# Kernel tuning notes

Measured on AMD Instinct MI355X. Metric: run time of the kernel, lower is better.

The kernel has to match this reference:

```python
import jax, jax.numpy as jnp
import numpy as np

N_NODES = 100000
N_EDGES = 1600000
IN_DIM, HID_DIM, OUT_DIM = 128, 64, 40


def setup_inputs() -> dict:
    key = jax.random.key(0)
    k1, k2, k3, k4, k5, k6 = jax.random.split(key, 6)
    x = jax.random.normal(k1, (N_NODES, IN_DIM), dtype=jnp.float32)
    edge_index = jax.random.randint(k2, (2, N_EDGES), 0, N_NODES, dtype=jnp.int64)
    W1 = jax.random.normal(k3, (IN_DIM, HID_DIM), dtype=jnp.float32) * 0.05
    b1 = jnp.zeros((HID_DIM,), dtype=jnp.float32)
    W2 = jax.random.normal(k4, (HID_DIM, OUT_DIM), dtype=jnp.float32) * 0.05
    b2 = jnp.zeros((OUT_DIM,), dtype=jnp.float32)
    return {"x": x, "edge_index": edge_index, "W1": W1, "b1": b1, "W2": W2, "b2": b2}


def gcn_conv(x, src, dst, W, b, n_nodes):
    """PyG GCNConv: linear -> symmetric-normalized aggregation (with self loops) -> + bias."""
    h = x @ W                                                # [N, C_out]
    # degree of targets, including the implicit self loop (weight 1 each)
    deg = jax.ops.segment_sum(jnp.ones_like(dst, dtype=h.dtype), dst,
                              num_segments=n_nodes) + 1.0    # [N]
    dinv = jax.lax.rsqrt(deg)                                # deg >= 1, always valid
    norm = dinv[src] * dinv[dst]                             # [E] edge norm coefficients
    msg = h[src] * norm[:, None]                             # [E, C_out] gather + scale
    agg = jax.ops.segment_sum(msg, dst, num_segments=n_nodes)
    # self-loop contribution: norm_ii = dinv_i * dinv_i
    agg = agg + h * (dinv * dinv)[:, None]
    return agg + b


def reference(x, edge_index, W1, b1, W2, b2):
    src, dst = edge_index[0], edge_index[1]  # source_to_target flow (PyG default)
    n = x.shape[0]
    h = gcn_conv(x, src, dst, W1, b1, n)
    h = jax.nn.relu(h)
    # dropout is identity in eval mode (training=False)
    out = gcn_conv(h, src, dst, W2, b2, n)
    return out
```

## Files before the change

kernel.cpp:

```cpp
#include <hip/hip_runtime.h>
#include <math.h>

#define N_NODES 100000
#define N_EDGES 1600000
#define IN_DIM 128
#define HID_DIM 64
#define OUT_DIM 40

#define NPAD 102400

#define BUCKET_SHIFT 7
#define BUCKET_NODES 128
#define N_BUCKETS 782
#define CHUNK 2048
#define N_CHUNKS 784

typedef _Float16 f16;
typedef _Float16 f16x2 __attribute__((ext_vector_type(2)));
typedef _Float16 f16x4 __attribute__((ext_vector_type(4)));
typedef _Float16 f16x8 __attribute__((ext_vector_type(8)));
typedef float f32x4 __attribute__((ext_vector_type(4)));


__global__ __launch_bounds__(256) void hist_kernel(const int* __restrict__ dst,
                                                   int* __restrict__ hist,
                                                   const float* __restrict__ W1,
                                                   const float* __restrict__ W2,
                                                   f16* __restrict__ w1f,
                                                   f16* __restrict__ w2f) {
    __shared__ int lh[N_BUCKETS];
    int c = blockIdx.x;
    int t = threadIdx.x;
    if (c < N_CHUNKS) {
        for (int b = t; b < N_BUCKETS; b += 256) lh[b] = 0;
        __syncthreads();
        int e0 = c * CHUNK;
        for (int i = t; i < CHUNK; i += 256) {
            int e = e0 + i;
            if (e < N_EDGES) atomicAdd(&lh[dst[e] >> BUCKET_SHIFT], 1);
        }
        __syncthreads();
        for (int b = t; b < N_BUCKETS; b += 256) hist[b * N_CHUNKS + c] = lh[b];
    } else if (c == N_CHUNKS) {
        for (int g = t; g < 1024; g += 256) {
            int f = g >> 6, L = g & 63;
            int s = f >> 2, cc = f & 3;
            int q = L >> 4, n = L & 15;
            f16x8 v;
#pragma unroll
            for (int j = 0; j < 8; ++j)
                v[j] = (f16)W1[(32 * s + 8 * q + j) * HID_DIM + 16 * cc + n];
            *(f16x8*)&w1f[(size_t)g * 8] = v;
        }
    } else {
        for (int g = t; g < 384; g += 256) {
            int f = g >> 6, L = g & 63;
            int s = f / 3, cc = f % 3;
            int q = L >> 4, n = L & 15;
            int col = 16 * cc + n;
            f16x8 v;
#pragma unroll
            for (int j = 0; j < 8; ++j)
                v[j] = (col < OUT_DIM) ? (f16)W2[(32 * s + 8 * q + j) * OUT_DIM + col] : (f16)0.f;
            *(f16x8*)&w2f[(size_t)g * 8] = v;
        }
    }
}

__global__ __launch_bounds__(256) void scan_chunks_kernel(const int* __restrict__ hist,
                                                          int* __restrict__ base,
                                                          int* __restrict__ bucketTotal) {
    __shared__ int lds[256];
    int b = blockIdx.x;
    int t = threadIdx.x;
    int v[4];
    int s = 0;
    for (int k = 0; k < 4; ++k) {
        int c = 4 * t + k;
        int cv = (c < N_CHUNKS) ? hist[b * N_CHUNKS + c] : 0;
        v[k] = s;
        s += cv;
    }
    lds[t] = s;
    __syncthreads();
    for (int off = 1; off < 256; off <<= 1) {
        int val = (t >= off) ? lds[t - off] : 0;
        __syncthreads();
        lds[t] += val;
        __syncthreads();
    }
    int excl = (t == 0) ? 0 : lds[t - 1];
    for (int k = 0; k < 4; ++k) {
        int c = 4 * t + k;
        if (c < N_CHUNKS) base[b * N_CHUNKS + c] = excl + v[k];
    }
    if (t == 255) bucketTotal[b] = lds[255];
}

__global__ __launch_bounds__(256) void scan_buckets_kernel(const int* __restrict__ bucketTotal,
                                                           int* __restrict__ bucketBase) {
    __shared__ int lds[256];
    int t = threadIdx.x;
    int v[4];
    int s = 0;
    for (int k = 0; k < 4; ++k) {
        int b = 4 * t + k;
        int cv = (b < N_BUCKETS) ? bucketTotal[b] : 0;
        v[k] = s;
        s += cv;
    }
    lds[t] = s;
    __syncthreads();
    for (int off = 1; off < 256; off <<= 1) {
        int val = (t >= off) ? lds[t - off] : 0;
        __syncthreads();
        lds[t] += val;
        __syncthreads();
    }
    int excl = (t == 0) ? 0 : lds[t - 1];
    for (int k = 0; k < 4; ++k) {
        int b = 4 * t + k;
        if (b < N_BUCKETS) bucketBase[b] = excl + v[k];
    }
}

__global__ __launch_bounds__(256) void scatter_kernel(const int* __restrict__ src,
                                                      const int* __restrict__ dst,
                                                      const int* __restrict__ base,
                                                      const int* __restrict__ bucketBase,
                                                      int* __restrict__ stage) {
    __shared__ int lbase[N_BUCKETS];
    __shared__ int lcnt[N_BUCKETS];
    int bid = blockIdx.x;
    int chunk = (bid & 7) * 98 + (bid >> 3);
    int t = threadIdx.x;
    for (int b = t; b < N_BUCKETS; b += 256) {
        lbase[b] = base[b * N_CHUNKS + chunk] + bucketBase[b];
        lcnt[b] = 0;
    }
    __syncthreads();
    int e0 = chunk * CHUNK;
    for (int i = t; i < CHUNK; i += 256) {
        int e = e0 + i;
        if (e < N_EDGES) {
            int d = dst[e];
            int b = d >> BUCKET_SHIFT;
            int pos = lbase[b] + atomicAdd(&lcnt[b], 1);
            stage[pos] = ((d & (BUCKET_NODES - 1)) << 17) | src[e];
        }
    }
}

__global__ __launch_bounds__(256) void place_kernel(const int* __restrict__ stage,
                                                    const int* __restrict__ bucketBase,
                                                    int* __restrict__ csr,
                                                    int* __restrict__ row_start,
                                                    int* __restrict__ cnt,
                                                    float* __restrict__ dinv) {
    __shared__ int lhist[BUCKET_NODES];
    __shared__ int lscan[BUCKET_NODES];
    __shared__ int lstart[BUCKET_NODES];
    __shared__ int lcur[BUCKET_NODES];
    int b = blockIdx.x;
    int t = threadIdx.x;
    int est = bucketBase[b];
    int een = (b == N_BUCKETS - 1) ? N_EDGES : bucketBase[b + 1];
    if (t < BUCKET_NODES) { lhist[t] = 0; lcur[t] = 0; }
    __syncthreads();
    for (int e = est + t; e < een; e += 256) atomicAdd(&lhist[stage[e] >> 17], 1);
    __syncthreads();
    if (t < BUCKET_NODES) lscan[t] = lhist[t];
    __syncthreads();
    for (int off = 1; off < BUCKET_NODES; off <<= 1) {
        int val = (t >= off && t < BUCKET_NODES) ? lscan[t - off] : 0;
        __syncthreads();
        if (t < BUCKET_NODES) lscan[t] += val;
        __syncthreads();
    }
    if (t < BUCKET_NODES) {
        int myexcl = (t == 0) ? 0 : lscan[t - 1];
        lstart[t] = est + myexcl;
        int node = (b << BUCKET_SHIFT) + t;
        if (node < N_NODES) {
            row_start[node] = est + myexcl;
            cnt[node] = lhist[t];
            dinv[node] = rsqrtf((float)lhist[t] + 1.0f);
        }
    }
    __syncthreads();
    for (int e = est + t; e < een; e += 256) {
        int rec = stage[e];
        int dl = rec >> 17;
        int pos = lstart[dl] + atomicAdd(&lcur[dl], 1);
        csr[pos] = rec & 0x1FFFF;
    }
}

__global__ __launch_bounds__(256) void gemm1_kernel(const float* __restrict__ x,
                                                    const f16* __restrict__ w1f,
                                                    const float* __restrict__ dinv,
                                                    f16* __restrict__ h1p) {
    __shared__ f16 aT[1088 * 8];
    int t = threadIdx.x;
    int nodeBase = blockIdx.x * 64;
    int L = t & 63;

    const f16x8* w1f8 = (const f16x8*)w1f;
    f16x8 bfrag[16];
#pragma unroll
    for (int f = 0; f < 16; ++f) bfrag[f] = w1f8[f * 64 + L];

#pragma unroll
    for (int i = 0; i < 8; ++i) {
        int idx = i * 256 + t;
        int node = idx >> 5;
        int col4 = idx & 31;
        int gnode = nodeBase + node;
        if (gnode >= N_NODES) gnode = N_NODES - 1;
        float4 v = *(const float4*)&x[(size_t)gnode * IN_DIM + col4 * 4];
        int w = node >> 4, m = node & 15;
        int s = col4 >> 3, q = (col4 >> 1) & 3, j0 = (col4 & 1) * 4;
        f16x4 h;
        h.x = (f16)v.x; h.y = (f16)v.y; h.z = (f16)v.z; h.w = (f16)v.w;
        int idx16 = (w * 4 + s) * 68 + 17 * q + m;
        *(f16x4*)&aT[idx16 * 8 + j0] = h;
    }
    __syncthreads();

    int wv = t >> 6;
    int q = L >> 4, m = L & 15;
    f32x4 acc[4] = {};
#pragma unroll
    for (int s = 0; s < 4; ++s) {
        f16x8 afrag = *(const f16x8*)&aT[((wv * 4 + s) * 68 + 17 * q + m) * 8];
#pragma unroll
        for (int c = 0; c < 4; ++c)
            acc[c] = __builtin_amdgcn_mfma_f32_16x16x32_f16(afrag, bfrag[s * 4 + c], acc[c], 0, 0, 0);
    }

#pragma unroll
    for (int r = 0; r < 4; ++r) {
        int node = nodeBase + 16 * wv + q * 4 + r;
        if (node < N_NODES) {
            float di = dinv[node];
#pragma unroll
            for (int c = 0; c < 4; ++c)
                h1p[(size_t)node * HID_DIM + 16 * c + m] = (f16)(acc[c][r] * di);
        }
    }
}

#define ZSTR 72
__global__ __launch_bounds__(256) void agg1mm_kernel(const f16* __restrict__ h1p,
                                                     const int* __restrict__ csr,
                                                     const int* __restrict__ row_start,
                                                     const int* __restrict__ cnt,
                                                     const float* __restrict__ dinv,
                                                     const float* __restrict__ b1,
                                                     const f16* __restrict__ w2f,
                                                     f16* __restrict__ h2p) {
    __shared__ f16 zT[64 * ZSTR];
    int t = threadIdx.x;
    int nodeBase = blockIdx.x * 64;
    int wv = t >> 6;
    int L = t & 63;
    int g = L >> 3;
    int s = L & 7;
    const f16x8* h8 = (const f16x8*)h1p;
    float bb[8];
#pragma unroll
    for (int j = 0; j < 8; ++j) bb[j] = b1[8 * s + j];

    for (int p = 0; p < 2; ++p) {
        int nodeLocal = 16 * wv + 8 * p + g;
        int node = nodeBase + nodeLocal;
        float acc[8];
#pragma unroll
        for (int j = 0; j < 8; ++j) acc[j] = 0.f;
        int lim = 0;
        const int* cp = csr;
        bool valid = (node < N_NODES);
        if (valid) {
            f16x8 sv = h8[(size_t)node * 8 + s];
#pragma unroll
            for (int j = 0; j < 8; ++j) acc[j] = (float)sv[j];
            lim = cnt[node];
            cp = csr + row_start[node];
        }
        for (int k = 0; k < lim; k += 8) {
            int ii[8]; float mm[8];
#pragma unroll
            for (int u = 0; u < 8; ++u) {
                int kk = k + u;
                bool ok = (kk < lim);
                ii[u] = cp[ok ? kk : k];
                mm[u] = ok ? 1.f : 0.f;
            }
            f16x8 f[8];
#pragma unroll
            for (int u = 0; u < 8; ++u) f[u] = h8[(size_t)ii[u] * 8 + s];
#pragma unroll
            for (int j = 0; j < 8; ++j) {
                float t0 = 0.f;
#pragma unroll
                for (int u = 0; u < 8; ++u) t0 += mm[u] * (float)f[u][j];
                acc[j] += t0;
            }
        }
        f16x8 o;
        if (valid) {
            float di = dinv[node];
#pragma unroll
            for (int j = 0; j < 8; ++j) {
                float v = acc[j] * di + bb[j];
                o[j] = (f16)(v > 0.f ? v : 0.f);
            }
        } else {
#pragma unroll
            for (int j = 0; j < 8; ++j) o[j] = (f16)0.f;
        }
        *(f16x8*)&zT[nodeLocal * ZSTR + 8 * s] = o;
    }
    __syncthreads();

    int q = L >> 4, m = L & 15;
    const f16x8* w2f8 = (const f16x8*)w2f;
    f32x4 acc2[3] = {};
#pragma unroll
    for (int ks = 0; ks < 2; ++ks) {
        f16x8 afrag = *(const f16x8*)&zT[(16 * wv + m) * ZSTR + 32 * ks + 8 * q];
#pragma unroll
        for (int c = 0; c < 3; ++c)
            acc2[c] = __builtin_amdgcn_mfma_f32_16x16x32_f16(afrag, w2f8[(ks * 3 + c) * 64 + L], acc2[c], 0, 0, 0);
    }
#pragma unroll
    for (int r = 0; r < 4; ++r) {
        int node = nodeBase + 16 * wv + q * 4 + r;
        if (node < N_NODES) {
            float di = dinv[node];
            h2p[(size_t)node * OUT_DIM + m]      = (f16)(acc2[0][r] * di);
            h2p[(size_t)node * OUT_DIM + 16 + m] = (f16)(acc2[1][r] * di);
            if (m < 8)
                h2p[(size_t)node * OUT_DIM + 32 + m] = (f16)(acc2[2][r] * di);
        }
    }
}

__global__ __launch_bounds__(256) void agg2_kernel(const f16* __restrict__ h2p,
                                                   const int* __restrict__ csr,
                                                   const int* __restrict__ row_start,
                                                   const int* __restrict__ cnt,
                                                   const float* __restrict__ dinv,
                                                   const float* __restrict__ b2,
                                                   float* __restrict__ out) {
    int t = threadIdx.x;
    int L = t & 63;
    int wv = t >> 6;
    int g = (L * 13) >> 6;
    int s = L - 5 * g;
    int node = blockIdx.x * 48 + wv * 12 + g;
    if (g >= 12 || node >= N_NODES) return;
    const f16x8* h8 = (const f16x8*)h2p;
    float acc[8];
    {
        f16x8 sv = h8[(size_t)node * 5 + s];
#pragma unroll
        for (int j = 0; j < 8; ++j) acc[j] = (float)sv[j];
    }
    int lim = cnt[node];
    const int* cp = csr + row_start[node];
    for (int k = 0; k < lim; k += 8) {
        int ii[8]; float mm[8];
#pragma unroll
        for (int u = 0; u < 8; ++u) {
            int kk = k + u;
            bool ok = (kk < lim);
            ii[u] = cp[ok ? kk : k];
            mm[u] = ok ? 1.f : 0.f;
        }
        f16x8 f[8];
#pragma unroll
        for (int u = 0; u < 8; ++u) f[u] = h8[(size_t)ii[u] * 5 + s];
#pragma unroll
        for (int j = 0; j < 8; ++j) {
            float t0 = 0.f;
#pragma unroll
            for (int u = 0; u < 8; ++u) t0 += mm[u] * (float)f[u][j];
            acc[j] += t0;
        }
    }
    float di = dinv[node];
    float4 o0, o1;
    o0.x = acc[0] * di + b2[8 * s + 0];
    o0.y = acc[1] * di + b2[8 * s + 1];
    o0.z = acc[2] * di + b2[8 * s + 2];
    o0.w = acc[3] * di + b2[8 * s + 3];
    o1.x = acc[4] * di + b2[8 * s + 4];
    o1.y = acc[5] * di + b2[8 * s + 5];
    o1.z = acc[6] * di + b2[8 * s + 6];
    o1.w = acc[7] * di + b2[8 * s + 7];
    *(float4*)&out[(size_t)node * OUT_DIM + 8 * s] = o0;
    *(float4*)&out[(size_t)node * OUT_DIM + 8 * s + 4] = o1;
}

extern "C" void kernel_launch(void* const* d_in, const int* in_sizes, int n_in,
                              void* d_out, int out_size, void* d_ws, size_t ws_size,
                              hipStream_t stream) {
    const float* x  = (const float*)d_in[0];
    const int*   ei = (const int*)d_in[1];
    const float* W1 = (const float*)d_in[2];
    const float* b1 = (const float*)d_in[3];
    const float* W2 = (const float*)d_in[4];
    const float* b2 = (const float*)d_in[5];
    float* out = (float*)d_out;

    const int* src = ei;
    const int* dst = ei + N_EDGES;

    int* wsi        = (int*)d_ws;
    int* hist       = wsi;
    int* base       = hist + N_BUCKETS * N_CHUNKS;
    int* bucketTotal= base + N_BUCKETS * N_CHUNKS;
    int* bucketBase = bucketTotal + 1024;
    int* row_start  = bucketBase + 1024;
    int* cnt        = row_start + NPAD;
    int* csr        = cnt + NPAD;
    int* stage      = csr + N_EDGES;
    float* dinv     = (float*)(stage + N_EDGES);
    f16*   h1p      = (f16*)(dinv + NPAD);
    f16*   h2p      = h1p + (size_t)N_NODES * HID_DIM;
    f16*   w1f      = h2p + (size_t)N_NODES * OUT_DIM;
    f16*   w2f      = w1f + 8192;

    hist_kernel<<<N_CHUNKS + 2, 256, 0, stream>>>(dst, hist, W1, W2, w1f, w2f);
    scan_chunks_kernel<<<N_BUCKETS, 256, 0, stream>>>(hist, base, bucketTotal);
    scan_buckets_kernel<<<1, 256, 0, stream>>>(bucketTotal, bucketBase);
    scatter_kernel<<<N_CHUNKS, 256, 0, stream>>>(src, dst, base, bucketBase, stage);
    place_kernel<<<N_BUCKETS, 256, 0, stream>>>(stage, bucketBase, csr, row_start, cnt, dinv);
    gemm1_kernel<<<(N_NODES + 63) / 64, 256, 0, stream>>>(x, w1f, dinv, h1p);
    agg1mm_kernel<<<(N_NODES + 63) / 64, 256, 0, stream>>>(h1p, csr, row_start, cnt, dinv, b1, w2f, h2p);
    agg2_kernel<<<(N_NODES + 47) / 48, 256, 0, stream>>>(h2p, csr, row_start, cnt, dinv, b2, out);
}
```

Before: 211.9 us.

## Sort CSR buckets in LDS with bitonic sort and pad h2 rows to 64

Buckets shrink from 128 to 64 nodes. Each bucket of at most 2048 edges is loaded into shared memory and bitonic-sorted by (local dst, src), so the CSR rows come out in deterministic, src-ascending order, which should improve gather locality in the aggregation kernels. The h2 intermediate is padded from 40 to 64 halves per row so each row is 128-byte aligned for the agg2 gathers. The costs are a full 2048-element bitonic network per bucket with many barriers, twice as many buckets (which enlarges the chunk histogram and scan work), and more memory traffic for the padded h2.

Result: slower. 297.2 us (+40.3%).

```diff
diff --git a/kernel.cpp b/kernel.cpp
--- a/kernel.cpp
+++ b/kernel.cpp
@@ -9,11 +9,12 @@
 
 #define NPAD 102400
 
-#define BUCKET_SHIFT 7
-#define BUCKET_NODES 128
-#define N_BUCKETS 782
+#define BUCKET_SHIFT 6
+#define BUCKET_NODES 64
+#define N_BUCKETS 1563
 #define CHUNK 2048
 #define N_CHUNKS 784
+#define SORT_N 2048
 
 typedef _Float16 f16;
 typedef _Float16 f16x2 __attribute__((ext_vector_type(2)));
@@ -101,10 +102,10 @@
                                                            int* __restrict__ bucketBase) {
     __shared__ int lds[256];
     int t = threadIdx.x;
-    int v[4];
+    int v[7];
     int s = 0;
-    for (int k = 0; k < 4; ++k) {
-        int b = 4 * t + k;
+    for (int k = 0; k < 7; ++k) {
+        int b = 7 * t + k;
         int cv = (b < N_BUCKETS) ? bucketTotal[b] : 0;
         v[k] = s;
         s += cv;
@@ -118,8 +119,8 @@
         __syncthreads();
     }
     int excl = (t == 0) ? 0 : lds[t - 1];
-    for (int k = 0; k < 4; ++k) {
-        int b = 4 * t + k;
+    for (int k = 0; k < 7; ++k) {
+        int b = 7 * t + k;
         if (b < N_BUCKETS) bucketBase[b] = excl + v[k];
     }
 }
@@ -157,6 +158,7 @@
                                                     int* __restrict__ row_start,
                                                     int* __restrict__ cnt,
                                                     float* __restrict__ dinv) {
+    __shared__ int keys[SORT_N];
     __shared__ int lhist[BUCKET_NODES];
     __shared__ int lscan[BUCKET_NODES];
     __shared__ int lstart[BUCKET_NODES];
@@ -165,9 +167,19 @@
     int t = threadIdx.x;
     int est = bucketBase[b];
     int een = (b == N_BUCKETS - 1) ? N_EDGES : bucketBase[b + 1];
+    int seg = een - est;
+    bool sorted_path = (seg <= SORT_N);
     if (t < BUCKET_NODES) { lhist[t] = 0; lcur[t] = 0; }
-    __syncthreads();
-    for (int e = est + t; e < een; e += 256) atomicAdd(&lhist[stage[e] >> 17], 1);
+    if (sorted_path) {
+        for (int i = t; i < SORT_N; i += 256)
+            keys[i] = (i < seg) ? stage[est + i] : 0x7FFFFFFF;
+    }
+    __syncthreads();
+    if (sorted_path) {
+        for (int i = t; i < seg; i += 256) atomicAdd(&lhist[keys[i] >> 17], 1);
+    } else {
+        for (int e = est + t; e < een; e += 256) atomicAdd(&lhist[stage[e] >> 17], 1);
+    }
     __syncthreads();
     if (t < BUCKET_NODES) lscan[t] = lhist[t];
     __syncthreads();
@@ -187,12 +199,30 @@
             dinv[node] = rsqrtf((float)lhist[t] + 1.0f);
         }
     }
-    __syncthreads();
-    for (int e = est + t; e < een; e += 256) {
-        int rec = stage[e];
-        int dl = rec >> 17;
-        int pos = lstart[dl] + atomicAdd(&lcur[dl], 1);
-        csr[pos] = rec & 0x1FFFF;
+    if (sorted_path) {
+        for (int kk = 2; kk <= SORT_N; kk <<= 1) {
+            for (int j = kk >> 1; j > 0; j >>= 1) {
+                __syncthreads();
+                for (int i = t; i < SORT_N; i += 256) {
+                    int l = i ^ j;
+                    if (l > i) {
+                        int a = keys[i], c2 = keys[l];
+                        bool up = ((i & kk) == 0);
+                        if ((a > c2) == up) { keys[i] = c2; keys[l] = a; }
+                    }
+                }
+            }
+        }
+        __syncthreads();
+        for (int i = t; i < seg; i += 256) csr[est + i] = keys[i] & 0x1FFFF;
+    } else {
+        __syncthreads();
+        for (int e = est + t; e < een; e += 256) {
+            int rec = stage[e];
+            int dl = rec >> 17;
+            int pos = lstart[dl] + atomicAdd(&lcur[dl], 1);
+            csr[pos] = rec & 0x1FFFF;
+        }
     }
 }
 
@@ -251,6 +281,7 @@
 }
 
 #define ZSTR 72
+#define H2STR 64
 __global__ __launch_bounds__(256) void agg1mm_kernel(const f16* __restrict__ h1p,
                                                      const int* __restrict__ csr,
                                                      const int* __restrict__ row_start,
@@ -338,10 +369,10 @@
         int node = nodeBase + 16 * wv + q * 4 + r;
         if (node < N_NODES) {
             float di = dinv[node];
-            h2p[(size_t)node * OUT_DIM + m]      = (f16)(acc2[0][r] * di);
-            h2p[(size_t)node * OUT_DIM + 16 + m] = (f16)(acc2[1][r] * di);
+            h2p[(size_t)node * H2STR + m]      = (f16)(acc2[0][r] * di);
+            h2p[(size_t)node * H2STR + 16 + m] = (f16)(acc2[1][r] * di);
             if (m < 8)
-                h2p[(size_t)node * OUT_DIM + 32 + m] = (f16)(acc2[2][r] * di);
+                h2p[(size_t)node * H2STR + 32 + m] = (f16)(acc2[2][r] * di);
         }
     }
 }
@@ -363,7 +394,7 @@
     const f16x8* h8 = (const f16x8*)h2p;
     float acc[8];
     {
-        f16x8 sv = h8[(size_t)node * 5 + s];
+        f16x8 sv = h8[(size_t)node * 8 + s];
 #pragma unroll
         for (int j = 0; j < 8; ++j) acc[j] = (float)sv[j];
     }
@@ -380,7 +411,7 @@
         }
         f16x8 f[8];
 #pragma unroll
-        for (int u = 0; u < 8; ++u) f[u] = h8[(size_t)ii[u] * 5 + s];
+        for (int u = 0; u < 8; ++u) f[u] = h8[(size_t)ii[u] * 8 + s];
 #pragma unroll
         for (int j = 0; j < 8; ++j) {
             float t0 = 0.f;
@@ -421,15 +452,15 @@
     int* hist       = wsi;
     int* base       = hist + N_BUCKETS * N_CHUNKS;
     int* bucketTotal= base + N_BUCKETS * N_CHUNKS;
-    int* bucketBase = bucketTotal + 1024;
-    int* row_start  = bucketBase + 1024;
+    int* bucketBase = bucketTotal + 2048;
+    int* row_start  = bucketBase + 2048;
     int* cnt        = row_start + NPAD;
     int* csr        = cnt + NPAD;
     int* stage      = csr + N_EDGES;
     float* dinv     = (float*)(stage + N_EDGES);
     f16*   h1p      = (f16*)(dinv + NPAD);
     f16*   h2p      = h1p + (size_t)N_NODES * HID_DIM;
-    f16*   w1f      = h2p + (size_t)N_NODES * OUT_DIM;
+    f16*   w1f      = h2p + (size_t)N_NODES * H2STR;
     f16*   w2f      = w1f + 8192;
 
     hist_kernel<<<N_CHUNKS + 2, 256, 0, stream>>>(dst, hist, W1, W2, w1f, w2f);
```

## Replace bucketed two-pass CSR build with global-atomic count/scan/scatter

Applied to the files above, without the earlier changes.

Replaces the bucketed histogram, two-level scan, staged scatter and per-bucket placement with a simpler CSR build. A per-node atomic count, a single-block 1024-thread scan over nodes, and a direct atomic scatter into CSR positions now fill the CSR. This removes two kernels and the staging buffer, but it relies on global atomics with random addresses and a serial single-block scan. Neighbor order within a row becomes nondeterministic. The h2 buffer is also padded to a 64-half stride so gathers in the second aggregation are 128-byte aligned.

Result: slower. 638.2 us (+201.2%).

```diff
diff --git a/kernel.cpp b/kernel.cpp
--- a/kernel.cpp
+++ b/kernel.cpp
@@ -8,40 +8,32 @@
 #define OUT_DIM 40
 
 #define NPAD 102400
-
-#define BUCKET_SHIFT 7
-#define BUCKET_NODES 128
-#define N_BUCKETS 782
-#define CHUNK 2048
-#define N_CHUNKS 784
+#define EBLK 1563
 
 typedef _Float16 f16;
-typedef _Float16 f16x2 __attribute__((ext_vector_type(2)));
 typedef _Float16 f16x4 __attribute__((ext_vector_type(4)));
 typedef _Float16 f16x8 __attribute__((ext_vector_type(8)));
 typedef float f32x4 __attribute__((ext_vector_type(4)));
 
 
-__global__ __launch_bounds__(256) void hist_kernel(const int* __restrict__ dst,
-                                                   int* __restrict__ hist,
-                                                   const float* __restrict__ W1,
-                                                   const float* __restrict__ W2,
-                                                   f16* __restrict__ w1f,
-                                                   f16* __restrict__ w2f) {
-    __shared__ int lh[N_BUCKETS];
-    int c = blockIdx.x;
-    int t = threadIdx.x;
-    if (c < N_CHUNKS) {
-        for (int b = t; b < N_BUCKETS; b += 256) lh[b] = 0;
-        __syncthreads();
-        int e0 = c * CHUNK;
-        for (int i = t; i < CHUNK; i += 256) {
-            int e = e0 + i;
-            if (e < N_EDGES) atomicAdd(&lh[dst[e] >> BUCKET_SHIFT], 1);
-        }
-        __syncthreads();
-        for (int b = t; b < N_BUCKETS; b += 256) hist[b * N_CHUNKS + c] = lh[b];
-    } else if (c == N_CHUNKS) {
+__global__ __launch_bounds__(256) void count_kernel(const int* __restrict__ dst,
+                                                    int* __restrict__ cnt,
+                                                    const float* __restrict__ W1,
+                                                    const float* __restrict__ W2,
+                                                    f16* __restrict__ w1f,
+                                                    f16* __restrict__ w2f) {
+    int bid = blockIdx.x;
+    int t = threadIdx.x;
+    if (bid < EBLK) {
+        int i = bid * 256 + t;
+        if (i < N_EDGES / 4) {
+            int4 d = ((const int4*)dst)[i];
+            atomicAdd(&cnt[d.x], 1);
+            atomicAdd(&cnt[d.y], 1);
+            atomicAdd(&cnt[d.z], 1);
+            atomicAdd(&cnt[d.w], 1);
+        }
+    } else if (bid == EBLK) {
         for (int g = t; g < 1024; g += 256) {
             int f = g >> 6, L = g & 63;
             int s = f >> 2, cc = f & 3;
@@ -67,133 +59,48 @@
     }
 }
 
-__global__ __launch_bounds__(256) void scan_chunks_kernel(const int* __restrict__ hist,
-                                                          int* __restrict__ base,
-                                                          int* __restrict__ bucketTotal) {
-    __shared__ int lds[256];
-    int b = blockIdx.x;
-    int t = threadIdx.x;
-    int v[4];
+#define SCAN_T 1024
+#define SCAN_PER 98
+__global__ __launch_bounds__(SCAN_T) void scan_kernel(const int* __restrict__ cnt,
+                                                      int* __restrict__ row_start,
+                                                      int* __restrict__ cur,
+                                                      float* __restrict__ dinv) {
+    __shared__ int lds[SCAN_T];
+    int t = threadIdx.x;
+    int n0 = t * SCAN_PER;
+    int n1 = n0 + SCAN_PER; if (n1 > N_NODES) n1 = N_NODES;
     int s = 0;
-    for (int k = 0; k < 4; ++k) {
-        int c = 4 * t + k;
-        int cv = (c < N_CHUNKS) ? hist[b * N_CHUNKS + c] : 0;
-        v[k] = s;
-        s += cv;
-    }
+    for (int n = n0; n < n1; ++n) s += cnt[n];
     lds[t] = s;
     __syncthreads();
-    for (int off = 1; off < 256; off <<= 1) {
+    for (int off = 1; off < SCAN_T; off <<= 1) {
         int val = (t >= off) ? lds[t - off] : 0;
         __syncthreads();
         lds[t] += val;
         __syncthreads();
     }
-    int excl = (t == 0) ? 0 : lds[t - 1];
-    for (int k = 0; k < 4; ++k) {
-        int c = 4 * t + k;
-        if (c < N_CHUNKS) base[b * N_CHUNKS + c] = excl + v[k];
-    }
-    if (t == 255) bucketTotal[b] = lds[255];
-}
-
-__global__ __launch_bounds__(256) void scan_buckets_kernel(const int* __restrict__ bucketTotal,
-                                                           int* __restrict__ bucketBase) {
-    __shared__ int lds[256];
-    int t = threadIdx.x;
-    int v[4];
-    int s = 0;
-    for (int k = 0; k < 4; ++k) {
-        int b = 4 * t + k;
-        int cv = (b < N_BUCKETS) ? bucketTotal[b] : 0;
-        v[k] = s;
-        s += cv;
-    }
-    lds[t] = s;
-    __syncthreads();
-    for (int off = 1; off < 256; off <<= 1) {
-        int val = (t >= off) ? lds[t - off] : 0;
-        __syncthreads();
-        lds[t] += val;
-        __syncthreads();
-    }
-    int excl = (t == 0) ? 0 : lds[t - 1];
-    for (int k = 0; k < 4; ++k) {
-        int b = 4 * t + k;
-        if (b < N_BUCKETS) bucketBase[b] = excl + v[k];
+    int running = (t == 0) ? 0 : lds[t - 1];
+    for (int n = n0; n < n1; ++n) {
+        int c = cnt[n];
+        row_start[n] = running;
+        cur[n] = running;
+        dinv[n] = rsqrtf((float)c + 1.0f);
+        running += c;
     }
 }
 
 __global__ __launch_bounds__(256) void scatter_kernel(const int* __restrict__ src,
                                                       const int* __restrict__ dst,
-                                                      const int* __restrict__ base,
-                                                      const int* __restrict__ bucketBase,
-                                                      int* __restrict__ stage) {
-    __shared__ int lbase[N_BUCKETS];
-    __shared__ int lcnt[N_BUCKETS];
-    int bid = blockIdx.x;
-    int chunk = (bid & 7) * 98 + (bid >> 3);
-    int t = threadIdx.x;
-    for (int b = t; b < N_BUCKETS; b += 256) {
-        lbase[b] = base[b * N_CHUNKS + chunk] + bucketBase[b];
-        lcnt[b] = 0;
-    }
-    __syncthreads();
-    int e0 = chunk * CHUNK;
-    for (int i = t; i < CHUNK; i += 256) {
-        int e = e0 + i;
-        if (e < N_EDGES) {
-            int d = dst[e];
-            int b = d >> BUCKET_SHIFT;
-            int pos = lbase[b] + atomicAdd(&lcnt[b], 1);
-            stage[pos] = ((d & (BUCKET_NODES - 1)) << 17) | src[e];
-        }
-    }
-}
-
-__global__ __launch_bounds__(256) void place_kernel(const int* __restrict__ stage,
-                                                    const int* __restrict__ bucketBase,
-                                                    int* __restrict__ csr,
-                                                    int* __restrict__ row_start,
-                                                    int* __restrict__ cnt,
-                                                    float* __restrict__ dinv) {
-    __shared__ int lhist[BUCKET_NODES];
-    __shared__ int lscan[BUCKET_NODES];
-    __shared__ int lstart[BUCKET_NODES];
-    __shared__ int lcur[BUCKET_NODES];
-    int b = blockIdx.x;
-    int t = threadIdx.x;
-    int est = bucketBase[b];
-    int een = (b == N_BUCKETS - 1) ? N_EDGES : bucketBase[b + 1];
-    if (t < BUCKET_NODES) { lhist[t] = 0; lcur[t] = 0; }
-    __syncthreads();
-    for (int e = est + t; e < een; e += 256) atomicAdd(&lhist[stage[e] >> 17], 1);
-    __syncthreads();
-    if (t < BUCKET_NODES) lscan[t] = lhist[t];
-    __syncthreads();
-    for (int off = 1; off < BUCKET_NODES; off <<= 1) {
-        int val = (t >= off && t < BUCKET_NODES) ? lscan[t - off] : 0;
-        __syncthreads();
-        if (t < BUCKET_NODES) lscan[t] += val;
-        __syncthreads();
-    }
-    if (t < BUCKET_NODES) {
-        int myexcl = (t == 0) ? 0 : lscan[t - 1];
-        lstart[t] = est + myexcl;
-        int node = (b << BUCKET_SHIFT) + t;
-        if (node < N_NODES) {
-            row_start[node] = est + myexcl;
-            cnt[node] = lhist[t];
-            dinv[node] = rsqrtf((float)lhist[t] + 1.0f);
-        }
-    }
-    __syncthreads();
-    for (int e = est + t; e < een; e += 256) {
-        int rec = stage[e];
-        int dl = rec >> 17;
-        int pos = lstart[dl] + atomicAdd(&lcur[dl], 1);
-        csr[pos] = rec & 0x1FFFF;
-    }
+                                                      int* __restrict__ cur,
+                                                      int* __restrict__ csr) {
+    int i = blockIdx.x * 256 + threadIdx.x;
+    if (i >= N_EDGES / 4) return;
+    int4 sv = ((const int4*)src)[i];
+    int4 dv = ((const int4*)dst)[i];
+    csr[atomicAdd(&cur[dv.x], 1)] = sv.x;
+    csr[atomicAdd(&cur[dv.y], 1)] = sv.y;
+    csr[atomicAdd(&cur[dv.z], 1)] = sv.z;
+    csr[atomicAdd(&cur[dv.w], 1)] = sv.w;
 }
 
 __global__ __launch_bounds__(256) void gemm1_kernel(const float* __restrict__ x,
@@ -251,6 +158,7 @@
 }
 
 #define ZSTR 72
+#define H2STR 64
 __global__ __launch_bounds__(256) void agg1mm_kernel(const f16* __restrict__ h1p,
                                                      const int* __restrict__ csr,
                                                      const int* __restrict__ row_start,
@@ -338,10 +246,10 @@
         int node = nodeBase + 16 * wv + q * 4 + r;
         if (node < N_NODES) {
             float di = dinv[node];
-            h2p[(size_t)node * OUT_DIM + m]      = (f16)(acc2[0][r] * di);
-            h2p[(size_t)node * OUT_DIM + 16 + m] = (f16)(acc2[1][r] * di);
+            h2p[(size_t)node * H2STR + m]      = (f16)(acc2[0][r] * di);
+            h2p[(size_t)node * H2STR + 16 + m] = (f16)(acc2[1][r] * di);
             if (m < 8)
-                h2p[(size_t)node * OUT_DIM + 32 + m] = (f16)(acc2[2][r] * di);
+                h2p[(size_t)node * H2STR + 32 + m] = (f16)(acc2[2][r] * di);
         }
     }
 }
@@ -363,7 +271,7 @@
     const f16x8* h8 = (const f16x8*)h2p;
     float acc[8];
     {
-        f16x8 sv = h8[(size_t)node * 5 + s];
+        f16x8 sv = h8[(size_t)node * 8 + s];
 #pragma unroll
         for (int j = 0; j < 8; ++j) acc[j] = (float)sv[j];
     }
@@ -380,7 +288,7 @@
         }
         f16x8 f[8];
 #pragma unroll
-        for (int u = 0; u < 8; ++u) f[u] = h8[(size_t)ii[u] * 5 + s];
+        for (int u = 0; u < 8; ++u) f[u] = h8[(size_t)ii[u] * 8 + s];
 #pragma unroll
         for (int j = 0; j < 8; ++j) {
             float t0 = 0.f;
@@ -418,25 +326,20 @@
     const int* dst = ei + N_EDGES;
 
     int* wsi        = (int*)d_ws;
-    int* hist       = wsi;
-    int* base       = hist + N_BUCKETS * N_CHUNKS;
-    int* bucketTotal= base + N_BUCKETS * N_CHUNKS;
-    int* bucketBase = bucketTotal + 1024;
-    int* row_start  = bucketBase + 1024;
+    int* row_start  = wsi;
     int* cnt        = row_start + NPAD;
-    int* csr        = cnt + NPAD;
-    int* stage      = csr + N_EDGES;
-    float* dinv     = (float*)(stage + N_EDGES);
+    int* cur        = cnt + NPAD;
+    int* csr        = cur + NPAD;
+    float* dinv     = (float*)(csr + N_EDGES);
     f16*   h1p      = (f16*)(dinv + NPAD);
     f16*   h2p      = h1p + (size_t)N_NODES * HID_DIM;
-    f16*   w1f      = h2p + (size_t)N_NODES * OUT_DIM;
+    f16*   w1f      = h2p + (size_t)N_NODES * H2STR;
     f16*   w2f      = w1f + 8192;
 
-    hist_kernel<<<N_CHUNKS + 2, 256, 0, stream>>>(dst, hist, W1, W2, w1f, w2f);
-    scan_chunks_kernel<<<N_BUCKETS, 256, 0, stream>>>(hist, base, bucketTotal);
-    scan_buckets_kernel<<<1, 256, 0, stream>>>(bucketTotal, bucketBase);
-    scatter_kernel<<<N_CHUNKS, 256, 0, stream>>>(src, dst, base, bucketBase, stage);
-    place_kernel<<<N_BUCKETS, 256, 0, stream>>>(stage, bucketBase, csr, row_start, cnt, dinv);
+    hipMemsetAsync(cnt, 0, N_NODES * sizeof(int), stream);
+    count_kernel<<<EBLK + 2, 256, 0, stream>>>(dst, cnt, W1, W2, w1f, w2f);
+    scan_kernel<<<1, SCAN_T, 0, stream>>>(cnt, row_start, cur, dinv);
+    scatter_kernel<<<EBLK, 256, 0, stream>>>(src, dst, cur, csr);
     gemm1_kernel<<<(N_NODES + 63) / 64, 256, 0, stream>>>(x, w1f, dinv, h1p);
     agg1mm_kernel<<<(N_NODES + 63) / 64, 256, 0, stream>>>(h1p, csr, row_start, cnt, dinv, b1, w2f, h2p);
     agg2_kernel<<<(N_NODES + 47) / 48, 256, 0, stream>>>(h2p, csr, row_start, cnt, dinv, b2, out);
```

## Enlarge edge chunks with vectorized int4 loads and pad h2 rows to 64

Applied to the files above, without the earlier changes.

The edge sort now uses fewer, larger chunks (8192 edges, 200 chunks) processed by 1024-thread blocks with int4 vectorized loads of src and dst. This shrinks the per-chunk histogram and base arrays and simplifies the chunk scan to one element per thread. The layer-2 feature buffer h2p is padded from 40 to 64 halves per row so each gathered row starts on a 128-byte boundary in agg2. The padding spends extra memory and write footprint, and the larger blocks may reduce occupancy or parallelism during the scatter phase.

Measured after the change: 198.6 us. 1.07x faster.

```diff
diff --git a/kernel.cpp b/kernel.cpp
--- a/kernel.cpp
+++ b/kernel.cpp
@@ -12,37 +12,45 @@
 #define BUCKET_SHIFT 7
 #define BUCKET_NODES 128
 #define N_BUCKETS 782
-#define CHUNK 2048
-#define N_CHUNKS 784
+#define CHUNK 8192
+#define N_CHUNKS 200
 
 typedef _Float16 f16;
-typedef _Float16 f16x2 __attribute__((ext_vector_type(2)));
 typedef _Float16 f16x4 __attribute__((ext_vector_type(4)));
 typedef _Float16 f16x8 __attribute__((ext_vector_type(8)));
 typedef float f32x4 __attribute__((ext_vector_type(4)));
 
 
-__global__ __launch_bounds__(256) void hist_kernel(const int* __restrict__ dst,
-                                                   int* __restrict__ hist,
-                                                   const float* __restrict__ W1,
-                                                   const float* __restrict__ W2,
-                                                   f16* __restrict__ w1f,
-                                                   f16* __restrict__ w2f) {
+__global__ __launch_bounds__(1024) void hist_kernel(const int* __restrict__ dst,
+                                                    int* __restrict__ hist,
+                                                    const float* __restrict__ W1,
+                                                    const float* __restrict__ W2,
+                                                    f16* __restrict__ w1f,
+                                                    f16* __restrict__ w2f) {
     __shared__ int lh[N_BUCKETS];
     int c = blockIdx.x;
     int t = threadIdx.x;
     if (c < N_CHUNKS) {
-        for (int b = t; b < N_BUCKETS; b += 256) lh[b] = 0;
-        __syncthreads();
-        int e0 = c * CHUNK;
-        for (int i = t; i < CHUNK; i += 256) {
-            int e = e0 + i;
-            if (e < N_EDGES) atomicAdd(&lh[dst[e] >> BUCKET_SHIFT], 1);
-        }
-        __syncthreads();
-        for (int b = t; b < N_BUCKETS; b += 256) hist[b * N_CHUNKS + c] = lh[b];
+        for (int b = t; b < N_BUCKETS; b += 1024) lh[b] = 0;
+        __syncthreads();
+        const int4* d4 = (const int4*)dst;
+        int i0 = c * (CHUNK / 4);
+#pragma unroll
+        for (int r = 0; r < 2; ++r) {
+            int idx = i0 + r * 1024 + t;
+            if (idx < N_EDGES / 4) {
+                int4 d = d4[idx];
+                atomicAdd(&lh[d.x >> BUCKET_SHIFT], 1);
+                atomicAdd(&lh[d.y >> BUCKET_SHIFT], 1);
+                atomicAdd(&lh[d.z >> BUCKET_SHIFT], 1);
+                atomicAdd(&lh[d.w >> BUCKET_SHIFT], 1);
+            }
+        }
+        __syncthreads();
+        for (int b = t; b < N_BUCKETS; b += 1024) hist[b * N_CHUNKS + c] = lh[b];
     } else if (c == N_CHUNKS) {
-        for (int g = t; g < 1024; g += 256) {
+        if (t < 1024) {
+            int g = t;
             int f = g >> 6, L = g & 63;
             int s = f >> 2, cc = f & 3;
             int q = L >> 4, n = L & 15;
@@ -53,7 +61,8 @@
             *(f16x8*)&w1f[(size_t)g * 8] = v;
         }
     } else {
-        for (int g = t; g < 384; g += 256) {
+        if (t < 384) {
+            int g = t;
             int f = g >> 6, L = g & 63;
             int s = f / 3, cc = f % 3;
             int q = L >> 4, n = L & 15;
@@ -73,15 +82,8 @@
     __shared__ int lds[256];
     int b = blockIdx.x;
     int t = threadIdx.x;
-    int v[4];
-    int s = 0;
-    for (int k = 0; k < 4; ++k) {
-        int c = 4 * t + k;
-        int cv = (c < N_CHUNKS) ? hist[b * N_CHUNKS + c] : 0;
-        v[k] = s;
-        s += cv;
-    }
-    lds[t] = s;
+    int cv = (t < N_CHUNKS) ? hist[b * N_CHUNKS + t] : 0;
+    lds[t] = cv;
     __syncthreads();
     for (int off = 1; off < 256; off <<= 1) {
         int val = (t >= off) ? lds[t - off] : 0;
@@ -89,11 +91,7 @@
         lds[t] += val;
         __syncthreads();
     }
-    int excl = (t == 0) ? 0 : lds[t - 1];
-    for (int k = 0; k < 4; ++k) {
-        int c = 4 * t + k;
-        if (c < N_CHUNKS) base[b * N_CHUNKS + c] = excl + v[k];
-    }
+    if (t < N_CHUNKS) base[b * N_CHUNKS + t] = lds[t] - cv;
     if (t == 255) bucketTotal[b] = lds[255];
 }
 
@@ -124,29 +122,43 @@
     }
 }
 
-__global__ __launch_bounds__(256) void scatter_kernel(const int* __restrict__ src,
-                                                      const int* __restrict__ dst,
-                                                      const int* __restrict__ base,
-                                                      const int* __restrict__ bucketBase,
-                                                      int* __restrict__ stage) {
+__global__ __launch_bounds__(1024) void scatter_kernel(const int* __restrict__ src,
+                                                       const int* __restrict__ dst,
+                                                       const int* __restrict__ base,
+                                                       const int* __restrict__ bucketBase,
+                                                       int* __restrict__ stage) {
     __shared__ int lbase[N_BUCKETS];
     __shared__ int lcnt[N_BUCKETS];
     int bid = blockIdx.x;
-    int chunk = (bid & 7) * 98 + (bid >> 3);
-    int t = threadIdx.x;
-    for (int b = t; b < N_BUCKETS; b += 256) {
+    int chunk = (bid & 7) * 25 + (bid >> 3);
+    int t = threadIdx.x;
+    for (int b = t; b < N_BUCKETS; b += 1024) {
         lbase[b] = base[b * N_CHUNKS + chunk] + bucketBase[b];
         lcnt[b] = 0;
     }
     __syncthreads();
-    int e0 = chunk * CHUNK;
-    for (int i = t; i < CHUNK; i += 256) {
-        int e = e0 + i;
-        if (e < N_EDGES) {
-            int d = dst[e];
-            int b = d >> BUCKET_SHIFT;
-            int pos = lbase[b] + atomicAdd(&lcnt[b], 1);
-            stage[pos] = ((d & (BUCKET_NODES - 1)) << 17) | src[e];
+    const int4* s4 = (const int4*)src;
+    const int4* d4 = (const int4*)dst;
+    int i0 = chunk * (CHUNK / 4);
+#pragma unroll
+    for (int r = 0; r < 2; ++r) {
+        int idx = i0 + r * 1024 + t;
+        if (idx < N_EDGES / 4) {
+            int4 sv = s4[idx];
+            int4 dv = d4[idx];
+            int d, b, pos;
+            d = dv.x; b = d >> BUCKET_SHIFT;
+            pos = lbase[b] + atomicAdd(&lcnt[b], 1);
+            stage[pos] = ((d & (BUCKET_NODES - 1)) << 17) | sv.x;
+            d = dv.y; b = d >> BUCKET_SHIFT;
+            pos = lbase[b] + atomicAdd(&lcnt[b], 1);
+            stage[pos] = ((d & (BUCKET_NODES - 1)) << 17) | sv.y;
+            d = dv.z; b = d >> BUCKET_SHIFT;
+            pos = lbase[b] + atomicAdd(&lcnt[b], 1);
+            stage[pos] = ((d & (BUCKET_NODES - 1)) << 17) | sv.z;
+            d = dv.w; b = d >> BUCKET_SHIFT;
+            pos = lbase[b] + atomicAdd(&lcnt[b], 1);
+            stage[pos] = ((d & (BUCKET_NODES - 1)) << 17) | sv.w;
         }
     }
 }
@@ -251,6 +263,7 @@
 }
 
 #define ZSTR 72
+#define H2STR 64
 __global__ __launch_bounds__(256) void agg1mm_kernel(const f16* __restrict__ h1p,
                                                      const int* __restrict__ csr,
                                                      const int* __restrict__ row_start,
@@ -338,10 +351,10 @@
         int node = nodeBase + 16 * wv + q * 4 + r;
         if (node < N_NODES) {
             float di = dinv[node];
-            h2p[(size_t)node * OUT_DIM + m]      = (f16)(acc2[0][r] * di);
-            h2p[(size_t)node * OUT_DIM + 16 + m] = (f16)(acc2[1][r] * di);
+            h2p[(size_t)node * H2STR + m]      = (f16)(acc2[0][r] * di);
+            h2p[(size_t)node * H2STR + 16 + m] = (f16)(acc2[1][r] * di);
             if (m < 8)
-                h2p[(size_t)node * OUT_DIM + 32 + m] = (f16)(acc2[2][r] * di);
+                h2p[(size_t)node * H2STR + 32 + m] = (f16)(acc2[2][r] * di);
         }
     }
 }
@@ -363,7 +376,7 @@
     const f16x8* h8 = (const f16x8*)h2p;
     float acc[8];
     {
-        f16x8 sv = h8[(size_t)node * 5 + s];
+        f16x8 sv = h8[(size_t)node * 8 + s];
 #pragma unroll
         for (int j = 0; j < 8; ++j) acc[j] = (float)sv[j];
     }
@@ -380,7 +393,7 @@
         }
         f16x8 f[8];
 #pragma unroll
-        for (int u = 0; u < 8; ++u) f[u] = h8[(size_t)ii[u] * 5 + s];
+        for (int u = 0; u < 8; ++u) f[u] = h8[(size_t)ii[u] * 8 + s];
 #pragma unroll
         for (int j = 0; j < 8; ++j) {
             float t0 = 0.f;
@@ -429,13 +442,13 @@
     float* dinv     = (float*)(stage + N_EDGES);
     f16*   h1p      = (f16*)(dinv + NPAD);
     f16*   h2p      = h1p + (size_t)N_NODES * HID_DIM;
-    f16*   w1f      = h2p + (size_t)N_NODES * OUT_DIM;
+    f16*   w1f      = h2p + (size_t)N_NODES * H2STR;
     f16*   w2f      = w1f + 8192;
 
-    hist_kernel<<<N_CHUNKS + 2, 256, 0, stream>>>(dst, hist, W1, W2, w1f, w2f);
+    hist_kernel<<<N_CHUNKS + 2, 1024, 0, stream>>>(dst, hist, W1, W2, w1f, w2f);
     scan_chunks_kernel<<<N_BUCKETS, 256, 0, stream>>>(hist, base, bucketTotal);
     scan_buckets_kernel<<<1, 256, 0, stream>>>(bucketTotal, bucketBase);
-    scatter_kernel<<<N_CHUNKS, 256, 0, stream>>>(src, dst, base, bucketBase, stage);
+    scatter_kernel<<<N_CHUNKS, 1024, 0, stream>>>(src, dst, base, bucketBase, stage);
     place_kernel<<<N_BUCKETS, 256, 0, stream>>>(stage, bucketBase, csr, row_start, cnt, dinv);
     gemm1_kernel<<<(N_NODES + 63) / 64, 256, 0, stream>>>(x, w1f, dinv, h1p);
     agg1mm_kernel<<<(N_NODES + 63) / 64, 256, 0, stream>>>(h1p, csr, row_start, cnt, dinv, b1, w2f, h2p);
```
